# Kernel optimization log

Measured on AMD Instinct MI355X. Metric: run time of the kernel, lower is better.

The kernel has to match this reference:

```python
import jax, jax.numpy as jnp
import numpy as np

N_NODES = 100000
HIDDEN = 128
N_EDGES = 1000000


def setup_inputs() -> dict:
    key = jax.random.key(0)
    k1, k2, k3, k4 = jax.random.split(key, 4)
    z = jax.random.normal(k1, (N_NODES, HIDDEN), dtype=jnp.float32)
    edge_label_index = jax.random.randint(k2, (2, N_EDGES), 0, N_NODES, dtype=jnp.int64)
    # Kaiming-ish scaled init for the two Linear layers (lin1: 2H->H, lin2: H->1)
    W1 = jax.random.normal(k3, (2 * HIDDEN, HIDDEN), dtype=jnp.float32) / np.sqrt(2 * HIDDEN)
    b1 = jnp.zeros((HIDDEN,), dtype=jnp.float32)
    W2 = jax.random.normal(k4, (HIDDEN, 1), dtype=jnp.float32) / np.sqrt(HIDDEN)
    b2 = jnp.zeros((1,), dtype=jnp.float32)
    return {"z": z, "edge_label_index": edge_label_index, "W1": W1, "b1": b1, "W2": W2, "b2": b2}


def reference(z, edge_label_index, W1, b1, W2, b2):
    row, col = edge_label_index[0], edge_label_index[1]
    # gather endpoint embeddings and concat: [E, 2H]
    h = jnp.concatenate([z[row], z[col]], axis=-1)
    h = jax.nn.relu(h @ W1 + b1)          # [E, H]
    out = h @ W2 + b2                     # [E, 1]
    return out.reshape(-1)
```

## Files before the change

kernel.cpp:

```cpp
#include <hip/hip_runtime.h>
#include <hip/hip_bf16.h>
#include <stdint.h>

#define HIDDEN 128
#define LDS_STRIDE 136

typedef __attribute__((ext_vector_type(8))) short short8;
typedef __attribute__((ext_vector_type(4))) unsigned uint4v;
typedef __attribute__((ext_vector_type(4))) float float4v;
typedef __attribute__((ext_vector_type(2))) float float2v;
typedef __attribute__((ext_vector_type(2))) unsigned uint2v;

static __device__ __forceinline__ unsigned short f2bf(float f) {
    union { float f; unsigned u; } v; v.f = f;
    unsigned r = (v.u + 0x7FFFu + ((v.u >> 16) & 1u)) >> 16;
    return (unsigned short)r;
}

static __device__ __forceinline__ unsigned pack2bf(float f0, float f1) {
    unsigned u0 = __float_as_uint(f0) + 0x8000u;
    unsigned u1 = __float_as_uint(f1) + 0x8000u;
    return __builtin_amdgcn_perm(u1, u0, 0x07060302u);
}

static __device__ __forceinline__ short8 pack8(float4v lo, float4v hi) {
    uint4v u;
    u[0] = pack2bf(lo[0], lo[1]);
    u[1] = pack2bf(lo[2], lo[3]);
    u[2] = pack2bf(hi[0], hi[1]);
    u[3] = pack2bf(hi[2], hi[3]);
    return *(short8*)&u;
}

__global__ void prep_wt(const float* __restrict__ W1, const float* __restrict__ b1,
                        const float* __restrict__ W2,
                        unsigned short* __restrict__ Wt,
                        float* __restrict__ b1p, float* __restrict__ W2p) {
    int idx = blockIdx.x * blockDim.x + threadIdx.x;
    if (idx < 256 * 128) {
        int j = idx >> 7, k = idx & 127;
        float v = (j < 128) ? W1[k * 128 + j] : W1[(128 + k) * 128 + (j - 128)];
        Wt[idx] = f2bf(v);
    }
    if (idx < 128) {
        int m = idx >> 3, tt = idx & 7;
        int jj = tt * 16 + m;
        b1p[idx] = b1[jj];
        W2p[idx] = W2[jj];
    }
}

__global__ __launch_bounds__(512) void node_gemm(
        const float* __restrict__ z, const unsigned short* __restrict__ Wt,
        const float* __restrict__ b1p,
        unsigned char* __restrict__ Qi, float* __restrict__ sA, float* __restrict__ sB,
        int n_nodes) {
    __shared__ unsigned short Wl[128 * LDS_STRIDE];

    int tid  = threadIdx.x;
    int h    = blockIdx.x & 1;

    #pragma unroll
    for (int i = 0; i < 4; ++i) {
        int chunk = tid + i * 512;
        int c  = chunk >> 4;
        int k0 = (chunk & 15) * 8;
        short8 v = *(const short8*)(Wt + h * 16384 + chunk * 8);
        *(short8*)(Wl + c * LDS_STRIDE + k0) = v;
    }
    __syncthreads();

    int lane = tid & 63;
    int wave = tid >> 6;
    int m    = lane & 15;
    int quad = lane >> 4;

    float4v b1a = (float4v)(0.0f), b1b = (float4v)(0.0f);
    if (h == 0) {
        b1a = *(const float4v*)(b1p + m * 8);
        b1b = *(const float4v*)(b1p + m * 8 + 4);
    }
    float* sArr = (h == 0) ? sA : sB;

    int nTiles = (n_nodes + 15) >> 4;
    int tileStride = (gridDim.x >> 1) * 8;

    for (int tile = (blockIdx.x >> 1) * 8 + wave; tile < nTiles; tile += tileStride) {
        int nodebase = tile * 16;
        int row = nodebase + m;

        short8 a[4];
        {
            bool ok = row < n_nodes;
            const float* zp = z + (size_t)row * HIDDEN + quad * 8;
            #pragma unroll
            for (int s = 0; s < 4; ++s) {
                float4v z0 = ok ? *(const float4v*)(zp + s * 32)     : (float4v)(0.0f);
                float4v z1 = ok ? *(const float4v*)(zp + s * 32 + 4) : (float4v)(0.0f);
                a[s] = pack8(z0, z1);
            }
        }

        float4v acc[8];
        #pragma unroll
        for (int t = 0; t < 8; ++t) acc[t] = (float4v)(0.0f);

        #pragma unroll
        for (int t = 0; t < 8; ++t) {
            const unsigned short* wp = Wl + (t * 16 + m) * LDS_STRIDE + quad * 8;
            #pragma unroll
            for (int s = 0; s < 4; ++s) {
                short8 b = *(const short8*)(wp + s * 32);
                acc[t] = __builtin_amdgcn_mfma_f32_16x16x32_bf16(a[s], b, acc[t], 0, 0, 0);
            }
        }

        #pragma unroll
        for (int r = 0; r < 4; ++r) {
            int node = nodebase + quad * 4 + r;
            float v[8];
            v[0] = acc[0][r] + b1a[0]; v[1] = acc[1][r] + b1a[1];
            v[2] = acc[2][r] + b1a[2]; v[3] = acc[3][r] + b1a[3];
            v[4] = acc[4][r] + b1b[0]; v[5] = acc[5][r] + b1b[1];
            v[6] = acc[6][r] + b1b[2]; v[7] = acc[7][r] + b1b[3];

            float amax = fabsf(v[0]);
            #pragma unroll
            for (int t = 1; t < 8; ++t) amax = fmaxf(amax, fabsf(v[t]));
            amax = fmaxf(amax, __shfl_xor(amax, 1));
            amax = fmaxf(amax, __shfl_xor(amax, 2));
            amax = fmaxf(amax, __shfl_xor(amax, 4));
            amax = fmaxf(amax, __shfl_xor(amax, 8));
            amax = fmaxf(amax, 1e-30f);

            float inv = 126.5f * __builtin_amdgcn_rcpf(amax);
            float s   = amax * (1.0f / 126.5f);

            unsigned d0 = 0, d1 = 0;
            #pragma unroll
            for (int t = 0; t < 4; ++t) {
                int q = (int)rintf(fmaf(v[t], inv, 128.0f));
                d0 |= ((unsigned)q & 255u) << (8 * t);
            }
            #pragma unroll
            for (int t = 0; t < 4; ++t) {
                int q = (int)rintf(fmaf(v[4 + t], inv, 128.0f));
                d1 |= ((unsigned)q & 255u) << (8 * t);
            }

            if (node < n_nodes) {
                uint2v pk; pk[0] = d0; pk[1] = d1;
                *(uint2v*)(Qi + (size_t)node * 256 + h * 128 + m * 8) = pk;
                if (m == 0) sArr[node] = s;
            }
        }
    }
}

__global__ __launch_bounds__(256) void edge_kernel(
        const int* __restrict__ eli, const unsigned char* __restrict__ Qi,
        const float* __restrict__ sA, const float* __restrict__ sB,
        const float* __restrict__ W2p, const float* __restrict__ b2,
        float* __restrict__ out, int E) {
    int g      = threadIdx.x >> 4;
    int lane16 = threadIdx.x & 15;
    int j0 = lane16 * 8;

    float4v wA = *(const float4v*)(W2p + j0);
    float4v wB = *(const float4v*)(W2p + j0 + 4);
    float bias2 = b2[0];

    int e0 = blockIdx.x * 64 + g;

    int idx_r[4], idx_c[4];
    #pragma unroll
    for (int i = 0; i < 4; ++i) {
        int e = e0 + i * 16;
        idx_r[i] = (e < E) ? eli[e]     : 0;
        idx_c[i] = (e < E) ? eli[E + e] : 0;
    }

    uint2v u1[4], u2[4];
    float s1[4], s2[4];
    #pragma unroll
    for (int i = 0; i < 4; ++i) {
        u1[i] = *(const uint2v*)(Qi + (size_t)idx_r[i] * 256 + j0);
        u2[i] = *(const uint2v*)(Qi + (size_t)idx_c[i] * 256 + 128 + j0);
        s1[i] = sA[idx_r[i]];
        s2[i] = sB[idx_c[i]];
    }

    #pragma unroll
    for (int i = 0; i < 4; ++i) {
        float a1 = s1[i], a2 = s2[i];
        float off = -128.0f * (a1 + a2);
        float acc = 0.0f;
        unsigned da = u1[i][0], db = u2[i][0];
        #pragma unroll
        for (int k = 0; k < 4; ++k) {
            float af = (float)((da >> (8 * k)) & 255u);
            float bf = (float)((db >> (8 * k)) & 255u);
            float v = fmaf(a2, bf, fmaf(a1, af, off));
            v = fmaxf(v, 0.0f);
            acc = fmaf(v, wA[k], acc);
        }
        da = u1[i][1]; db = u2[i][1];
        #pragma unroll
        for (int k = 0; k < 4; ++k) {
            float af = (float)((da >> (8 * k)) & 255u);
            float bf = (float)((db >> (8 * k)) & 255u);
            float v = fmaf(a2, bf, fmaf(a1, af, off));
            v = fmaxf(v, 0.0f);
            acc = fmaf(v, wB[k], acc);
        }

        acc += __shfl_xor(acc, 1);
        acc += __shfl_xor(acc, 2);
        acc += __shfl_xor(acc, 4);
        acc += __shfl_xor(acc, 8);

        int e = e0 + i * 16;
        if (lane16 == 0 && e < E) out[e] = acc + bias2;
    }
}

extern "C" void kernel_launch(void* const* d_in, const int* in_sizes, int n_in,
                              void* d_out, int out_size, void* d_ws, size_t ws_size,
                              hipStream_t stream) {
    const float* z   = (const float*)d_in[0];
    const int*   eli = (const int*)d_in[1];
    const float* W1  = (const float*)d_in[2];
    const float* b1  = (const float*)d_in[3];
    const float* W2  = (const float*)d_in[4];
    const float* b2  = (const float*)d_in[5];
    int n_nodes = in_sizes[0] / HIDDEN;
    int E       = in_sizes[1] / 2;
    float* out  = (float*)d_out;

    size_t off = 0;
    unsigned char* Qi  = (unsigned char*)d_ws;              off += (size_t)n_nodes * 256;
    unsigned short* Wt = (unsigned short*)((char*)d_ws + off); off += 256 * 128 * 2;
    float* b1p = (float*)((char*)d_ws + off);               off += 128 * 4;
    float* W2p = (float*)((char*)d_ws + off);               off += 128 * 4;
    float* sA  = (float*)((char*)d_ws + off);               off += (size_t)n_nodes * 4;
    float* sB  = (float*)((char*)d_ws + off);               off += (size_t)n_nodes * 4;

    prep_wt<<<128, 256, 0, stream>>>(W1, b1, W2, Wt, b1p, W2p);

    node_gemm<<<1024, 512, 0, stream>>>(z, Wt, b1p, Qi, sA, sB, n_nodes);

    edge_kernel<<<(E + 63) / 64, 256, 0, stream>>>(eli, Qi, sA, sB, W2p, b2, out, E);
}
```

Before: 163.0 us.

## Bucket-sort edges by endpoint node ranges for cache-local gathers

```diff
diff --git a/kernel.cpp b/kernel.cpp
--- a/kernel.cpp
+++ b/kernel.cpp
@@ -35,8 +35,14 @@
 __global__ void prep_wt(const float* __restrict__ W1, const float* __restrict__ b1,
                         const float* __restrict__ W2,
                         unsigned short* __restrict__ Wt,
-                        float* __restrict__ b1p, float* __restrict__ W2p) {
-    int idx = blockIdx.x * blockDim.x + threadIdx.x;
+                        float* __restrict__ b1p, float* __restrict__ W2p,
+                        const int* __restrict__ eli, int E, unsigned M,
+                        int* __restrict__ cnt) {
+    __shared__ int hh[64];
+    int t = threadIdx.x;
+    if (t < 64) hh[t] = 0;
+
+    int idx = blockIdx.x * blockDim.x + t;
     if (idx < 256 * 128) {
         int j = idx >> 7, k = idx & 127;
         float v = (j < 128) ? W1[k * 128 + j] : W1[(128 + k) * 128 + (j - 128)];
@@ -47,6 +53,56 @@
         int jj = tt * 16 + m;
         b1p[idx] = b1[jj];
         W2p[idx] = W2[jj];
+    }
+    __syncthreads();
+    for (int i = idx; i < E; i += gridDim.x * blockDim.x) {
+        int r = eli[i], c = eli[E + i];
+        int b = (int)(__umulhi((unsigned)r, M) * 8 + __umulhi((unsigned)c, M));
+        atomicAdd(&hh[b], 1);
+    }
+    __syncthreads();
+    if (t < 64 && hh[t] > 0) atomicAdd(&cnt[t], hh[t]);
+}
+
+__global__ void bucket_scan(const int* __restrict__ cnt, int* __restrict__ boff,
+                            int* __restrict__ cur) {
+    if (threadIdx.x == 0) {
+        int acc = 0;
+        for (int i = 0; i < 64; ++i) { boff[i] = acc; cur[i] = acc; acc += cnt[i]; }
+        boff[64] = acc;
+    }
+}
+
+__global__ void edge_scatter(const int* __restrict__ eli, int E, unsigned M,
+                             int* __restrict__ cur, int* __restrict__ sr,
+                             unsigned long long* __restrict__ sce) {
+    __shared__ int hh[64];
+    __shared__ int base[64];
+    const int CH = 2048;
+    int t = threadIdx.x;
+    int start = blockIdx.x * CH;
+    if (start >= E) return;
+    int end = min(start + CH, E);
+
+    if (t < 64) hh[t] = 0;
+    __syncthreads();
+    for (int i = start + t; i < end; i += 256) {
+        int r = eli[i], c = eli[E + i];
+        int b = (int)(__umulhi((unsigned)r, M) * 8 + __umulhi((unsigned)c, M));
+        atomicAdd(&hh[b], 1);
+    }
+    __syncthreads();
+    if (t < 64) {
+        base[t] = (hh[t] > 0) ? atomicAdd(&cur[t], hh[t]) : 0;
+        hh[t] = 0;
+    }
+    __syncthreads();
+    for (int i = start + t; i < end; i += 256) {
+        int r = eli[i], c = eli[E + i];
+        int b = (int)(__umulhi((unsigned)r, M) * 8 + __umulhi((unsigned)c, M));
+        int p = base[b] + atomicAdd(&hh[b], 1);
+        sr[p]  = r;
+        sce[p] = ((unsigned long long)(unsigned)i << 32) | (unsigned)c;
     }
 }
 
@@ -153,6 +209,90 @@
                 *(uint2v*)(Qi + (size_t)node * 256 + h * 128 + m * 8) = pk;
                 if (m == 0) sArr[node] = s;
             }
+        }
+    }
+}
+
+static __device__ __forceinline__ float edge_dot8(uint2v u1, uint2v u2,
+                                                  float a1, float a2,
+                                                  float4v wA, float4v wB) {
+    float off = -128.0f * (a1 + a2);
+    float acc = 0.0f;
+    unsigned da = u1[0], db = u2[0];
+    #pragma unroll
+    for (int k = 0; k < 4; ++k) {
+        float af = (float)((da >> (8 * k)) & 255u);
+        float bf = (float)((db >> (8 * k)) & 255u);
+        float v = fmaf(a2, bf, fmaf(a1, af, off));
+        v = fmaxf(v, 0.0f);
+        acc = fmaf(v, wA[k], acc);
+    }
+    da = u1[1]; db = u2[1];
+    #pragma unroll
+    for (int k = 0; k < 4; ++k) {
+        float af = (float)((da >> (8 * k)) & 255u);
+        float bf = (float)((db >> (8 * k)) & 255u);
+        float v = fmaf(a2, bf, fmaf(a1, af, off));
+        v = fmaxf(v, 0.0f);
+        acc = fmaf(v, wB[k], acc);
+    }
+    return acc;
+}
+
+__global__ __launch_bounds__(256) void edge_kernel_b(
+        const int* __restrict__ sr, const unsigned long long* __restrict__ sce,
+        const int* __restrict__ boff,
+        const unsigned char* __restrict__ Qi,
+        const float* __restrict__ sA, const float* __restrict__ sB,
+        const float* __restrict__ W2p, const float* __restrict__ b2,
+        float* __restrict__ out) {
+    int g      = threadIdx.x >> 4;
+    int lane16 = threadIdx.x & 15;
+    int j0 = lane16 * 8;
+
+    float4v wA = *(const float4v*)(W2p + j0);
+    float4v wB = *(const float4v*)(W2p + j0 + 4);
+    float bias2 = b2[0];
+
+    int x  = blockIdx.x & 7;
+    int kb = blockIdx.x >> 3;
+    int K  = gridDim.x >> 3;
+    int rs = boff[x * 8];
+    int re = boff[x * 8 + 8];
+
+    for (int base = rs + kb * 64; base < re; base += K * 64) {
+        int idx_r[4], idx_c[4], oe[4];
+        bool okf[4];
+        #pragma unroll
+        for (int i = 0; i < 4; ++i) {
+            int e = base + i * 16 + g;
+            bool ok = e < re;
+            okf[i] = ok;
+            int ee = ok ? e : base;
+            idx_r[i] = sr[ee];
+            unsigned long long ce = sce[ee];
+            idx_c[i] = (int)(unsigned)(ce & 0xFFFFFFFFull);
+            oe[i]    = (int)(unsigned)(ce >> 32);
+        }
+
+        uint2v u1[4], u2[4];
+        float s1[4], s2[4];
+        #pragma unroll
+        for (int i = 0; i < 4; ++i) {
+            u1[i] = *(const uint2v*)(Qi + (size_t)idx_r[i] * 256 + j0);
+            u2[i] = *(const uint2v*)(Qi + (size_t)idx_c[i] * 256 + 128 + j0);
+            s1[i] = sA[idx_r[i]];
+            s2[i] = sB[idx_c[i]];
+        }
+
+        #pragma unroll
+        for (int i = 0; i < 4; ++i) {
+            float acc = edge_dot8(u1[i], u2[i], s1[i], s2[i], wA, wB);
+            acc += __shfl_xor(acc, 1);
+            acc += __shfl_xor(acc, 2);
+            acc += __shfl_xor(acc, 4);
+            acc += __shfl_xor(acc, 8);
+            if (lane16 == 0 && okf[i]) out[oe[i]] = acc + bias2;
         }
     }
 }
@@ -192,33 +332,11 @@
 
     #pragma unroll
     for (int i = 0; i < 4; ++i) {
-        float a1 = s1[i], a2 = s2[i];
-        float off = -128.0f * (a1 + a2);
-        float acc = 0.0f;
-        unsigned da = u1[i][0], db = u2[i][0];
-        #pragma unroll
-        for (int k = 0; k < 4; ++k) {
-            float af = (float)((da >> (8 * k)) & 255u);
-            float bf = (float)((db >> (8 * k)) & 255u);
-            float v = fmaf(a2, bf, fmaf(a1, af, off));
-            v = fmaxf(v, 0.0f);
-            acc = fmaf(v, wA[k], acc);
-        }
-        da = u1[i][1]; db = u2[i][1];
-        #pragma unroll
-        for (int k = 0; k < 4; ++k) {
-            float af = (float)((da >> (8 * k)) & 255u);
-            float bf = (float)((db >> (8 * k)) & 255u);
-            float v = fmaf(a2, bf, fmaf(a1, af, off));
-            v = fmaxf(v, 0.0f);
-            acc = fmaf(v, wB[k], acc);
-        }
-
+        float acc = edge_dot8(u1[i], u2[i], s1[i], s2[i], wA, wB);
         acc += __shfl_xor(acc, 1);
         acc += __shfl_xor(acc, 2);
         acc += __shfl_xor(acc, 4);
         acc += __shfl_xor(acc, 8);
-
         int e = e0 + i * 16;
         if (lane16 == 0 && e < E) out[e] = acc + bias2;
     }
@@ -237,17 +355,34 @@
     int E       = in_sizes[1] / 2;
     float* out  = (float*)d_out;
 
+    unsigned M = (unsigned)((((unsigned long long)8 << 32) + n_nodes - 1) / (unsigned)n_nodes);
+
     size_t off = 0;
-    unsigned char* Qi  = (unsigned char*)d_ws;              off += (size_t)n_nodes * 256;
+    unsigned char* Qi  = (unsigned char*)d_ws;                 off += (size_t)n_nodes * 256;
     unsigned short* Wt = (unsigned short*)((char*)d_ws + off); off += 256 * 128 * 2;
-    float* b1p = (float*)((char*)d_ws + off);               off += 128 * 4;
-    float* W2p = (float*)((char*)d_ws + off);               off += 128 * 4;
-    float* sA  = (float*)((char*)d_ws + off);               off += (size_t)n_nodes * 4;
-    float* sB  = (float*)((char*)d_ws + off);               off += (size_t)n_nodes * 4;
-
-    prep_wt<<<128, 256, 0, stream>>>(W1, b1, W2, Wt, b1p, W2p);
-
-    node_gemm<<<1024, 512, 0, stream>>>(z, Wt, b1p, Qi, sA, sB, n_nodes);
-
-    edge_kernel<<<(E + 63) / 64, 256, 0, stream>>>(eli, Qi, sA, sB, W2p, b2, out, E);
-}
+    float* b1p = (float*)((char*)d_ws + off);                  off += 128 * 4;
+    float* W2p = (float*)((char*)d_ws + off);                  off += 128 * 4;
+    float* sA  = (float*)((char*)d_ws + off);                  off += (size_t)n_nodes * 4;
+    float* sB  = (float*)((char*)d_ws + off);                  off += (size_t)n_nodes * 4;
+    off = (off + 255) & ~(size_t)255;
+    int* sr  = (int*)((char*)d_ws + off);                      off += (size_t)E * 4;
+    off = (off + 7) & ~(size_t)7;
+    unsigned long long* sce = (unsigned long long*)((char*)d_ws + off); off += (size_t)E * 8;
+    int* cnt  = (int*)((char*)d_ws + off);                     off += 64 * 4;
+    int* boff = (int*)((char*)d_ws + off);                     off += 65 * 4;
+    int* cur  = (int*)((char*)d_ws + off);                     off += 64 * 4;
+    bool use_sort = (off <= ws_size);
+
+    if (use_sort) {
+        hipMemsetAsync(cnt, 0, 64 * 4, stream);
+        prep_wt<<<128, 256, 0, stream>>>(W1, b1, W2, Wt, b1p, W2p, eli, E, M, cnt);
+        bucket_scan<<<1, 64, 0, stream>>>(cnt, boff, cur);
+        edge_scatter<<<(E + 2047) / 2048, 256, 0, stream>>>(eli, E, M, cur, sr, sce);
+        node_gemm<<<1024, 512, 0, stream>>>(z, Wt, b1p, Qi, sA, sB, n_nodes);
+        edge_kernel_b<<<2048, 256, 0, stream>>>(sr, sce, boff, Qi, sA, sB, W2p, b2, out);
+    } else {
+        prep_wt<<<128, 256, 0, stream>>>(W1, b1, W2, Wt, b1p, W2p, eli, 0, M, (int*)Qi);
+        node_gemm<<<1024, 512, 0, stream>>>(z, Wt, b1p, Qi, sA, sB, n_nodes);
+        edge_kernel<<<(E + 63) / 64, 256, 0, stream>>>(eli, Qi, sA, sB, W2p, b2, out, E);
+    }
+}
```

Result: slower. 191.6 us (+17.5%).

## Launch one tile per wave in node GEMM, prefetch z before weight staging

Applied to the files above, without the earlier changes.

```diff
diff --git a/kernel.cpp b/kernel.cpp
--- a/kernel.cpp
+++ b/kernel.cpp
@@ -59,6 +59,27 @@
 
     int tid  = threadIdx.x;
     int h    = blockIdx.x & 1;
+    int lane = tid & 63;
+    int wave = tid >> 6;
+    int m    = lane & 15;
+    int quad = lane >> 4;
+
+    int nTiles   = (n_nodes + 15) >> 4;
+    int tile     = (blockIdx.x >> 1) * 8 + wave;
+    bool active  = tile < nTiles;
+    int nodebase = tile * 16;
+    int row      = nodebase + m;
+
+    float4v zr[8];
+    {
+        bool ok = active && (row < n_nodes);
+        const float* zp = z + (size_t)row * HIDDEN + quad * 8;
+        #pragma unroll
+        for (int s = 0; s < 4; ++s) {
+            zr[2 * s]     = ok ? *(const float4v*)(zp + s * 32)     : (float4v)(0.0f);
+            zr[2 * s + 1] = ok ? *(const float4v*)(zp + s * 32 + 4) : (float4v)(0.0f);
+        }
+    }
 
     #pragma unroll
     for (int i = 0; i < 4; ++i) {
@@ -69,11 +90,7 @@
         *(short8*)(Wl + c * LDS_STRIDE + k0) = v;
     }
     __syncthreads();
-
-    int lane = tid & 63;
-    int wave = tid >> 6;
-    int m    = lane & 15;
-    int quad = lane >> 4;
+    if (!active) return;
 
     float4v b1a = (float4v)(0.0f), b1b = (float4v)(0.0f);
     if (h == 0) {
@@ -82,79 +99,91 @@
     }
     float* sArr = (h == 0) ? sA : sB;
 
-    int nTiles = (n_nodes + 15) >> 4;
-    int tileStride = (gridDim.x >> 1) * 8;
-
-    for (int tile = (blockIdx.x >> 1) * 8 + wave; tile < nTiles; tile += tileStride) {
-        int nodebase = tile * 16;
-        int row = nodebase + m;
-
-        short8 a[4];
-        {
-            bool ok = row < n_nodes;
-            const float* zp = z + (size_t)row * HIDDEN + quad * 8;
-            #pragma unroll
-            for (int s = 0; s < 4; ++s) {
-                float4v z0 = ok ? *(const float4v*)(zp + s * 32)     : (float4v)(0.0f);
-                float4v z1 = ok ? *(const float4v*)(zp + s * 32 + 4) : (float4v)(0.0f);
-                a[s] = pack8(z0, z1);
-            }
-        }
-
-        float4v acc[8];
-        #pragma unroll
-        for (int t = 0; t < 8; ++t) acc[t] = (float4v)(0.0f);
-
-        #pragma unroll
-        for (int t = 0; t < 8; ++t) {
-            const unsigned short* wp = Wl + (t * 16 + m) * LDS_STRIDE + quad * 8;
-            #pragma unroll
-            for (int s = 0; s < 4; ++s) {
-                short8 b = *(const short8*)(wp + s * 32);
-                acc[t] = __builtin_amdgcn_mfma_f32_16x16x32_bf16(a[s], b, acc[t], 0, 0, 0);
-            }
-        }
-
-        #pragma unroll
-        for (int r = 0; r < 4; ++r) {
-            int node = nodebase + quad * 4 + r;
-            float v[8];
-            v[0] = acc[0][r] + b1a[0]; v[1] = acc[1][r] + b1a[1];
-            v[2] = acc[2][r] + b1a[2]; v[3] = acc[3][r] + b1a[3];
-            v[4] = acc[4][r] + b1b[0]; v[5] = acc[5][r] + b1b[1];
-            v[6] = acc[6][r] + b1b[2]; v[7] = acc[7][r] + b1b[3];
-
-            float amax = fabsf(v[0]);
-            #pragma unroll
-            for (int t = 1; t < 8; ++t) amax = fmaxf(amax, fabsf(v[t]));
-            amax = fmaxf(amax, __shfl_xor(amax, 1));
-            amax = fmaxf(amax, __shfl_xor(amax, 2));
-            amax = fmaxf(amax, __shfl_xor(amax, 4));
-            amax = fmaxf(amax, __shfl_xor(amax, 8));
-            amax = fmaxf(amax, 1e-30f);
-
-            float inv = 126.5f * __builtin_amdgcn_rcpf(amax);
-            float s   = amax * (1.0f / 126.5f);
-
-            unsigned d0 = 0, d1 = 0;
-            #pragma unroll
-            for (int t = 0; t < 4; ++t) {
-                int q = (int)rintf(fmaf(v[t], inv, 128.0f));
-                d0 |= ((unsigned)q & 255u) << (8 * t);
-            }
-            #pragma unroll
-            for (int t = 0; t < 4; ++t) {
-                int q = (int)rintf(fmaf(v[4 + t], inv, 128.0f));
-                d1 |= ((unsigned)q & 255u) << (8 * t);
-            }
-
-            if (node < n_nodes) {
-                uint2v pk; pk[0] = d0; pk[1] = d1;
-                *(uint2v*)(Qi + (size_t)node * 256 + h * 128 + m * 8) = pk;
-                if (m == 0) sArr[node] = s;
-            }
-        }
-    }
+    short8 a[4];
+    #pragma unroll
+    for (int s = 0; s < 4; ++s) a[s] = pack8(zr[2 * s], zr[2 * s + 1]);
+
+    float4v acc[8];
+    #pragma unroll
+    for (int t = 0; t < 8; ++t) acc[t] = (float4v)(0.0f);
+
+    #pragma unroll
+    for (int t = 0; t < 8; ++t) {
+        const unsigned short* wp = Wl + (t * 16 + m) * LDS_STRIDE + quad * 8;
+        #pragma unroll
+        for (int s = 0; s < 4; ++s) {
+            short8 b = *(const short8*)(wp + s * 32);
+            acc[t] = __builtin_amdgcn_mfma_f32_16x16x32_bf16(a[s], b, acc[t], 0, 0, 0);
+        }
+    }
+
+    #pragma unroll
+    for (int r = 0; r < 4; ++r) {
+        int node = nodebase + quad * 4 + r;
+        float v[8];
+        v[0] = acc[0][r] + b1a[0]; v[1] = acc[1][r] + b1a[1];
+        v[2] = acc[2][r] + b1a[2]; v[3] = acc[3][r] + b1a[3];
+        v[4] = acc[4][r] + b1b[0]; v[5] = acc[5][r] + b1b[1];
+        v[6] = acc[6][r] + b1b[2]; v[7] = acc[7][r] + b1b[3];
+
+        float amax = fabsf(v[0]);
+        #pragma unroll
+        for (int t = 1; t < 8; ++t) amax = fmaxf(amax, fabsf(v[t]));
+        amax = fmaxf(amax, __shfl_xor(amax, 1));
+        amax = fmaxf(amax, __shfl_xor(amax, 2));
+        amax = fmaxf(amax, __shfl_xor(amax, 4));
+        amax = fmaxf(amax, __shfl_xor(amax, 8));
+        amax = fmaxf(amax, 1e-30f);
+
+        float inv = 126.5f * __builtin_amdgcn_rcpf(amax);
+        float s   = amax * (1.0f / 126.5f);
+
+        unsigned d0 = 0, d1 = 0;
+        #pragma unroll
+        for (int t = 0; t < 4; ++t) {
+            int q = (int)rintf(fmaf(v[t], inv, 128.0f));
+            d0 |= ((unsigned)q & 255u) << (8 * t);
+        }
+        #pragma unroll
+        for (int t = 0; t < 4; ++t) {
+            int q = (int)rintf(fmaf(v[4 + t], inv, 128.0f));
+            d1 |= ((unsigned)q & 255u) << (8 * t);
+        }
+
+        if (node < n_nodes) {
+            uint2v pk; pk[0] = d0; pk[1] = d1;
+            *(uint2v*)(Qi + (size_t)node * 256 + h * 128 + m * 8) = pk;
+            if (m == 0) sArr[node] = s;
+        }
+    }
+}
+
+static __device__ __forceinline__ float edge_dot8(uint2v u1, uint2v u2,
+                                                  float a1, float a2,
+                                                  const float2v* w2) {
+    float offs = -128.0f * (a1 + a2);
+    float2v off2; off2[0] = offs; off2[1] = offs;
+    float2v a1v;  a1v[0] = a1;   a1v[1] = a1;
+    float2v a2v;  a2v[0] = a2;   a2v[1] = a2;
+    float2v acc2; acc2[0] = 0.0f; acc2[1] = 0.0f;
+    #pragma unroll
+    for (int d = 0; d < 2; ++d) {
+        unsigned da = u1[d], db = u2[d];
+        #pragma unroll
+        for (int p = 0; p < 2; ++p) {
+            float2v af, bf;
+            af[0] = (float)((da >> (16 * p))     & 255u);
+            af[1] = (float)((da >> (16 * p + 8)) & 255u);
+            bf[0] = (float)((db >> (16 * p))     & 255u);
+            bf[1] = (float)((db >> (16 * p + 8)) & 255u);
+            float2v t = a2v * bf + off2;
+            float2v s = a1v * af + t;
+            s[0] = fmaxf(s[0], 0.0f);
+            s[1] = fmaxf(s[1], 0.0f);
+            acc2 = acc2 + s * w2[2 * d + p];
+        }
+    }
+    return acc2[0] + acc2[1];
 }
 
 __global__ __launch_bounds__(256) void edge_kernel(
@@ -166,8 +195,9 @@
     int lane16 = threadIdx.x & 15;
     int j0 = lane16 * 8;
 
-    float4v wA = *(const float4v*)(W2p + j0);
-    float4v wB = *(const float4v*)(W2p + j0 + 4);
+    float2v w2[4];
+    #pragma unroll
+    for (int k = 0; k < 4; ++k) w2[k] = ((const float2v*)(W2p + j0))[k];
     float bias2 = b2[0];
 
     int e0 = blockIdx.x * 64 + g;
@@ -192,35 +222,14 @@
 
     #pragma unroll
     for (int i = 0; i < 4; ++i) {
-        float a1 = s1[i], a2 = s2[i];
-        float off = -128.0f * (a1 + a2);
-        float acc = 0.0f;
-        unsigned da = u1[i][0], db = u2[i][0];
-        #pragma unroll
-        for (int k = 0; k < 4; ++k) {
-            float af = (float)((da >> (8 * k)) & 255u);
-            float bf = (float)((db >> (8 * k)) & 255u);
-            float v = fmaf(a2, bf, fmaf(a1, af, off));
-            v = fmaxf(v, 0.0f);
-            acc = fmaf(v, wA[k], acc);
-        }
-        da = u1[i][1]; db = u2[i][1];
-        #pragma unroll
-        for (int k = 0; k < 4; ++k) {
-            float af = (float)((da >> (8 * k)) & 255u);
-            float bf = (float)((db >> (8 * k)) & 255u);
-            float v = fmaf(a2, bf, fmaf(a1, af, off));
-            v = fmaxf(v, 0.0f);
-            acc = fmaf(v, wB[k], acc);
-        }
-
+        float acc = edge_dot8(u1[i], u2[i], s1[i], s2[i], w2);
         acc += __shfl_xor(acc, 1);
         acc += __shfl_xor(acc, 2);
         acc += __shfl_xor(acc, 4);
         acc += __shfl_xor(acc, 8);
-
         int e = e0 + i * 16;
-        if (lane16 == 0 && e < E) out[e] = acc + bias2;
+        if (lane16 == 0 && e < E)
+            __builtin_nontemporal_store(acc + bias2, &out[e]);
     }
 }
 
@@ -238,16 +247,18 @@
     float* out  = (float*)d_out;
 
     size_t off = 0;
-    unsigned char* Qi  = (unsigned char*)d_ws;              off += (size_t)n_nodes * 256;
+    unsigned char* Qi  = (unsigned char*)d_ws;                 off += (size_t)n_nodes * 256;
     unsigned short* Wt = (unsigned short*)((char*)d_ws + off); off += 256 * 128 * 2;
-    float* b1p = (float*)((char*)d_ws + off);               off += 128 * 4;
-    float* W2p = (float*)((char*)d_ws + off);               off += 128 * 4;
-    float* sA  = (float*)((char*)d_ws + off);               off += (size_t)n_nodes * 4;
-    float* sB  = (float*)((char*)d_ws + off);               off += (size_t)n_nodes * 4;
+    float* b1p = (float*)((char*)d_ws + off);                  off += 128 * 4;
+    float* W2p = (float*)((char*)d_ws + off);                  off += 128 * 4;
+    float* sA  = (float*)((char*)d_ws + off);                  off += (size_t)n_nodes * 4;
+    float* sB  = (float*)((char*)d_ws + off);                  off += (size_t)n_nodes * 4;
 
     prep_wt<<<128, 256, 0, stream>>>(W1, b1, W2, Wt, b1p, W2p);
 
-    node_gemm<<<1024, 512, 0, stream>>>(z, Wt, b1p, Qi, sA, sB, n_nodes);
+    int nTiles = (n_nodes + 15) / 16;
+    int blocksPerHalf = (nTiles + 7) / 8;
+    node_gemm<<<2 * blocksPerHalf, 512, 0, stream>>>(z, Wt, b1p, Qi, sA, sB, n_nodes);
 
     edge_kernel<<<(E + 63) / 64, 256, 0, stream>>>(eli, Qi, sA, sB, W2p, b2, out, E);
 }
```

Result: no change. 159.9 us (-1.9%).
